# Kernel optimization log

Hardware: AMD Instinct MI355X
Metric: run time of the kernel (lower is better)

Reference implementation:

```python
import jax, jax.numpy as jnp
import numpy as np

B, S, H, NH = 2, 2048, 1024, 16
HD = H // NH


def setup_inputs() -> dict:
    key = jax.random.key(0)
    ks = jax.random.split(key, 14)
    lim = 1.0 / np.sqrt(H)  # torch Linear default init range
    def lin(ka, kb):
        W = jax.random.uniform(ka, (H, H), jnp.float32, -lim, lim)
        b = jax.random.uniform(kb, (H,), jnp.float32, -lim, lim)
        return W, b
    Wq, bq = lin(ks[0], ks[1])
    Wk, bk = lin(ks[2], ks[3])
    Wv, bv = lin(ks[4], ks[5])
    Wo, bo = lin(ks[6], ks[7])
    return {
        "query": jax.random.normal(ks[8], (B, S, H), jnp.float32),
        "key": jax.random.normal(ks[9], (B, S, H), jnp.float32),
        "value": jax.random.normal(ks[10], (B, S, H), jnp.float32),
        "attn_mask": jax.random.randint(ks[11], (B, S, S), 0, 2).astype(bool),
        "relative_time": jax.random.normal(ks[12], (B, 1, S, S), jnp.float32),
        "Wq": Wq, "bq": bq, "Wk": Wk, "bk": bk,
        "Wv": Wv, "bv": bv, "Wo": Wo, "bo": bo,
    }


def reference(query, key, value, attn_mask, relative_time,
              Wq, bq, Wk, bk, Wv, bv, Wo, bo):
    Bq, Sq, _ = query.shape
    Skv = key.shape[1]
    # projections (torch Linear: x @ W^T + b)
    Q = (query @ Wq.T + bq).reshape(Bq, Sq, NH, HD).transpose(0, 2, 1, 3)
    K = (key @ Wk.T + bk).reshape(Bq, Skv, NH, HD).transpose(0, 2, 1, 3)
    V = (value @ Wv.T + bv).reshape(Bq, Skv, NH, HD).transpose(0, 2, 1, 3)
    scale = HD ** (-0.5)
    # NOTE: bias added BEFORE scaling, matching the original (non-standard)
    scores = jnp.einsum("bhqd,bhkd->bhqk", Q, K)
    scores = (scores + relative_time) * scale
    scores = jnp.where(attn_mask[:, None, :, :], scores, -jnp.inf)
    attn = jax.nn.softmax(scores.astype(jnp.float32), axis=-1).astype(scores.dtype)
    attn = jnp.nan_to_num(attn, nan=0.0)
    # dropout is identity in eval mode (dropout_rate applied only when training)
    out = jnp.einsum("bhqk,bhkd->bhqd", attn, V)
    out = out.transpose(0, 2, 1, 3).reshape(Bq, Sq, H)
    return out @ Wo.T + bo
```

## Files before the change

### kernel.cpp

```cpp
#include <hip/hip_runtime.h>
#include <hip/hip_bf16.h>

constexpr int BATCH = 2, SEQ = 2048, HDIM = 1024, NHEADS = 16, HEADD = 64;
constexpr int MROWS = BATCH * SEQ;
constexpr float QSCALE = 0.18033688011112042f;

typedef short short8  __attribute__((ext_vector_type(8)));
typedef float f32x4   __attribute__((ext_vector_type(4)));
typedef float f32x16  __attribute__((ext_vector_type(16)));
typedef int   int4v   __attribute__((ext_vector_type(4)));
typedef unsigned short ushort4v __attribute__((ext_vector_type(4)));

static __device__ __forceinline__ short f2bf(float f) {
    __hip_bfloat16 h = __float2bfloat16(f);
    return *reinterpret_cast<short*>(&h);
}

static __device__ __forceinline__ int cvt_pk_bf16(float a, float b) {
    int r;
    asm("v_cvt_pk_bf16_f32 %0, %1, %2" : "=v"(r) : "v"(a), "v"(b));
    return r;
}

static __device__ __forceinline__ float bfbits2f(unsigned short u) {
    return __builtin_bit_cast(float, (unsigned int)u << 16);
}

static __device__ __forceinline__ void gload_lds16(const void* g, void* l) {
    __builtin_amdgcn_global_load_lds(
        (const __attribute__((address_space(1))) unsigned int*)g,
        (__attribute__((address_space(3))) unsigned int*)l, 16, 0, 0);
}

static __device__ __forceinline__ int swz(int row) {
    return (((row & 7) ^ ((row >> 3) & 3))) << 4;
}

__global__ void cvt_all_kernel(const float* __restrict__ q, const float* __restrict__ k,
                               const float* __restrict__ v, const float* __restrict__ w0,
                               const float* __restrict__ w1, const float* __restrict__ w2,
                               const float* __restrict__ w3,
                               short* __restrict__ xq, short* __restrict__ xk,
                               short* __restrict__ xv, short* __restrict__ o0,
                               short* __restrict__ o1, short* __restrict__ o2,
                               short* __restrict__ o3, int n4x, int n4w) {
    int i = blockIdx.x * blockDim.x + threadIdx.x;
    const int stride = gridDim.x * blockDim.x;
    const int total = 3 * n4x + 4 * n4w;
    for (; i < total; i += stride) {
        const float* in; short* out; int j = i;
        if (j < 3 * n4x) {
            if (j >= 2 * n4x)      { in = v; out = xv; j -= 2 * n4x; }
            else if (j >= n4x)     { in = k; out = xk; j -= n4x; }
            else                   { in = q; out = xq; }
        } else {
            j -= 3 * n4x;
            if (j >= 3 * n4w)      { in = w3; out = o3; j -= 3 * n4w; }
            else if (j >= 2 * n4w) { in = w2; out = o2; j -= 2 * n4w; }
            else if (j >= n4w)     { in = w1; out = o1; j -= n4w; }
            else                   { in = w0; out = o0; }
        }
        const float4 val = reinterpret_cast<const float4*>(in)[j];
        short4 o;
        o.x = f2bf(val.x); o.y = f2bf(val.y); o.z = f2bf(val.z); o.w = f2bf(val.w);
        reinterpret_cast<short4*>(out)[j] = o;
    }
}

__global__ void detect_mask_kernel(const unsigned int* __restrict__ m, int* flag) {
    const int tid = threadIdx.x;
    int gt1 = 0, isf = 0;
    for (int i = 0; i < 4; ++i) {
        unsigned int wv = m[tid + 256 * i];
        if (wv > 1u) gt1 = 1;
        if (wv == 0x3F800000u) isf = 1;
    }
    __shared__ int s_gt1, s_isf;
    if (tid == 0) { s_gt1 = 0; s_isf = 0; }
    __syncthreads();
    if (gt1) atomicOr(&s_gt1, 1);
    if (isf) atomicOr(&s_isf, 1);
    __syncthreads();
    if (tid == 0) flag[0] = s_gt1 ? (s_isf ? 2 : 1) : 0;
}

__global__ void fuse_rel_kernel(const float* __restrict__ rel, const void* __restrict__ mask,
                                const int* __restrict__ flag, short* __restrict__ rT,
                                int nThr) {
    const int f = flag[0];
    int i = blockIdx.x * blockDim.x + threadIdx.x;
    const int stride = gridDim.x * blockDim.x;
    for (; i < nThr; i += stride) {
        const int q    = i & 2047;
        const int kv16 = (i >> 11) & 127;
        const int b    = i >> 18;
        const long base = ((long)(b * 2048 + q)) * 2048 + kv16 * 16;
        float4 rv[4];
        #pragma unroll
        for (int g = 0; g < 4; ++g)
            rv[g] = *reinterpret_cast<const float4*>(rel + base + 4 * g);
        bool mk[16];
        if (f == 1) {
            const unsigned int* mp = (const unsigned int*)((const unsigned char*)mask + base);
            #pragma unroll
            for (int wd = 0; wd < 4; ++wd) {
                const unsigned int mw = mp[wd];
                #pragma unroll
                for (int s = 0; s < 4; ++s) mk[wd * 4 + s] = ((mw >> (8 * s)) & 0xffu) != 0;
            }
        } else if (f == 0) {
            const int* mp = (const int*)mask + base;
            #pragma unroll
            for (int j = 0; j < 16; ++j) mk[j] = mp[j] != 0;
        } else {
            const float* mp = (const float*)mask + base;
            #pragma unroll
            for (int j = 0; j < 16; ++j) mk[j] = mp[j] != 0.0f;
        }
        const float* rp = reinterpret_cast<const float*>(&rv[0]);
        #pragma unroll
        for (int g = 0; g < 4; ++g) {
            short4 o;
            short* op = reinterpret_cast<short*>(&o);
            #pragma unroll
            for (int j = 0; j < 4; ++j) {
                const int idx = 4 * g + j;
                op[j] = f2bf(mk[idx] ? rp[idx] * QSCALE : -1e30f);
            }
            *reinterpret_cast<short4*>(rT + (((long)(b * 512 + kv16 * 4 + g)) * 2048 + q) * 4) = o;
        }
    }
}

template<int BN, typename EPI>
static __device__ __forceinline__
void gemm_core(const short* A, const short* Bw, int K, int m0, int n0, EPI epi) {
    constexpr int NFRAG = BN / 32;
    __shared__ short As[128 * 64];
    __shared__ short Bs[BN * 64];
    const int tid  = threadIdx.x;
    const int lane = tid & 63;
    const int w    = tid >> 6;
    const int lo   = lane & 15, hi = lane >> 4;
    const int wm   = w >> 1, wn = w & 1;

    f32x4 acc[4][NFRAG] = {};

    const int arow  = tid >> 3;
    const int acolb = (tid & 7) * 16;
    const int scolS = acolb ^ swz(arow);
    const char* Ab = (const char*)A + ((long)(m0 + arow) * K) * 2 + scolS;
    const char* Bb = (const char*)Bw + ((long)(n0 + arow) * K) * 2 + scolS;

    for (int k0 = 0; k0 < K; k0 += 64) {
        #pragma unroll
        for (int i = 0; i < 4; ++i)
            gload_lds16(Ab + ((long)i * 32 * K + k0) * 2, (char*)As + i * 4096 + tid * 16);
        #pragma unroll
        for (int i = 0; i < NFRAG; ++i)
            gload_lds16(Bb + ((long)i * 32 * K + k0) * 2, (char*)Bs + i * 4096 + tid * 16);
        __syncthreads();
        #pragma unroll
        for (int ks = 0; ks < 2; ++ks) {
            short8 af[4], bf[NFRAG];
            #pragma unroll
            for (int fm = 0; fm < 4; ++fm) {
                const int row = wm * 64 + fm * 16 + lo;
                af[fm] = *reinterpret_cast<const short8*>(
                    (const char*)As + row * 128 + ((ks * 64 + hi * 16) ^ swz(row)));
            }
            #pragma unroll
            for (int fn = 0; fn < NFRAG; ++fn) {
                const int row = wn * (BN / 2) + fn * 16 + lo;
                bf[fn] = *reinterpret_cast<const short8*>(
                    (const char*)Bs + row * 128 + ((ks * 64 + hi * 16) ^ swz(row)));
            }
            #pragma unroll
            for (int fm = 0; fm < 4; ++fm)
                #pragma unroll
                for (int fn = 0; fn < NFRAG; ++fn)
                    acc[fm][fn] = __builtin_amdgcn_mfma_f32_16x16x32_bf16(
                        af[fm], bf[fn], acc[fm][fn], 0, 0, 0);
        }
        __syncthreads();
    }

    #pragma unroll
    for (int fm = 0; fm < 4; ++fm)
        #pragma unroll
        for (int fn = 0; fn < NFRAG; ++fn) {
            const int n = n0 + wn * (BN / 2) + fn * 16 + lo;
            const int mB = m0 + wm * 64 + fm * 16 + hi * 4;
            for (int r = 0; r < 4; ++r) epi(mB + r, n, acc[fm][fn][r]);
        }
}

__global__ __launch_bounds__(256, 3)
void qkv_gemm(const short* xq, const short* xk, const short* xv,
              const short* wq, const short* wk, const short* wv,
              const float* bq, const float* bk, const float* bv,
              short* Qb, short* Kb, short* Vt) {
    const int which = blockIdx.x >> 8;
    const int bid   = blockIdx.x & 255;
    const int m0 = (bid >> 3) << 7;
    const int n0 = (bid & 7) << 7;
    const short* A    = which == 0 ? xq : which == 1 ? xk : xv;
    const short* W    = which == 0 ? wq : which == 1 ? wk : wv;
    const float* bias = which == 0 ? bq : which == 1 ? bk : bv;
    short* C          = which == 0 ? Qb : which == 1 ? Kb : Vt;
    const float scale = which == 0 ? QSCALE : 1.0f;
    gemm_core<128>(A, W, HDIM, m0, n0, [&](int m, int n, float v) {
        v = (v + bias[n]) * scale;
        const int b = m >> 11, s = m & (SEQ - 1);
        const int h = n >> 6, d = n & 63;
        long idx;
        if (which != 2) idx = (((long)(b * NHEADS + h)) * SEQ + s) * HEADD + d;
        else            idx = (((long)(b * NHEADS + h)) * HEADD + d) * SEQ + s;
        C[idx] = f2bf(v);
    });
}

__global__ __launch_bounds__(256, 2)
void out_gemm(const short* A, const short* W, const float* bias, float* Cout) {
    const int bid = blockIdx.x;
    const int m0 = (bid >> 4) << 7;
    const int n0 = (bid & 15) << 6;
    gemm_core<64>(A, W, HDIM, m0, n0, [&](int m, int n, float v) {
        Cout[(long)m * HDIM + n] = v + bias[n];
    });
}

__global__ __launch_bounds__(256, 4)
void attn_fwd(const short* __restrict__ Qb, const short* __restrict__ Kb,
              const short* __restrict__ Vtb, const short* __restrict__ rT,
              short* __restrict__ Ob) {
    __shared__ short Ks[2][64 * 64];
    __shared__ short Vs[2][64 * 64];
    const int tid  = threadIdx.x;
    const int lane = tid & 63;
    const int wv   = tid >> 6;
    const int qp   = wv & 1;
    const int t    = wv >> 1;
    const int l31  = lane & 31, hi2 = lane >> 5;
    const int wg = ((blockIdx.x & 7) << 7) + (blockIdx.x >> 3);
    const int qt = wg & 31, h = (wg >> 5) & 15, b = wg >> 9;
    const int bh = b * NHEADS + h;
    const int q0 = qt * 64 + qp * 32 + l31;

    short8 qf[4];
    {
        const short* qp_ = Qb + ((long)bh * SEQ + q0) * HEADD + hi2 * 8;
        #pragma unroll
        for (int s = 0; s < 4; ++s)
            qf[s] = *reinterpret_cast<const short8*>(qp_ + s * 16);
    }

    float lsum = 0.0f;
    f32x16 oacc0 = {}, oacc1 = {};

    const int srow  = tid >> 3;
    const int scolb = (tid & 7) * 16;
    const int scolK = scolb ^ swz(srow);
    const char* KbB = (const char*)Kb + ((long)bh * SEQ + srow) * 128 + scolK;
    const char* VbB = (const char*)Vtb + ((long)bh * HEADD + srow) * ((long)SEQ * 2) + scolK;

    auto stage = [&](int buf, int kt) {
        #pragma unroll
        for (int i = 0; i < 2; ++i) {
            gload_lds16(KbB + ((long)kt * 64 + i * 32) * 128,
                        (char*)&Ks[buf][0] + i * 4096 + tid * 16);
            gload_lds16(VbB + (long)i * 32 * (SEQ * 2) + (long)kt * 128,
                        (char*)&Vs[buf][0] + i * 4096 + tid * 16);
        }
    };

    ushort4v rbuf[4];
    auto loadRel = [&](int kt) {
        #pragma unroll
        for (int g = 0; g < 4; ++g) {
            const int p4 = kt * 16 + t * 8 + 2 * g + hi2;
            rbuf[g] = *reinterpret_cast<const ushort4v*>(
                rT + (((long)(b * 512 + p4)) * 2048 + q0) * 4);
        }
    };

    stage(0, 0);
    loadRel(0);

    const int rsw = swz(l31);
    const int NT = SEQ / 64;

    for (int kt = 0; kt < NT; ++kt) {
        const int cb = kt & 1;
        const bool hasNext = (kt < NT - 1);
        if (hasNext) stage(cb ^ 1, kt + 1);
        if (hasNext) asm volatile("s_waitcnt vmcnt(4)" ::: "memory");
        else         asm volatile("s_waitcnt vmcnt(0)" ::: "memory");
        __builtin_amdgcn_s_barrier();
        asm volatile("" ::: "memory");

        f32x16 sc;
        #pragma unroll
        for (int g = 0; g < 4; ++g)
            #pragma unroll
            for (int j = 0; j < 4; ++j)
                sc[4 * g + j] = bfbits2f(rbuf[g][j]);
        if (hasNext) loadRel(kt + 1);

        const char* kls = (const char*)&Ks[cb][0];
        const char* kr  = kls + (t * 32 + l31) * 128;
        __builtin_amdgcn_s_setprio(1);
        #pragma unroll
        for (int s = 0; s < 4; ++s) {
            short8 kf = *reinterpret_cast<const short8*>(kr + ((s * 32 + hi2 * 16) ^ rsw));
            sc = __builtin_amdgcn_mfma_f32_32x32x16_bf16(kf, qf[s], sc, 0, 0, 0);
        }
        __builtin_amdgcn_s_setprio(0);

        int X[8];
        #pragma unroll
        for (int i2 = 0; i2 < 8; ++i2) {
            const float p0 = __builtin_amdgcn_exp2f(sc[2 * i2]);
            const float p1 = __builtin_amdgcn_exp2f(sc[2 * i2 + 1]);
            lsum += p0 + p1;
            X[i2] = cvt_pk_bf16(p0, p1);
        }
        int pa[2][4];
        #pragma unroll
        for (int u = 0; u < 2; ++u) {
            auto r0 = __builtin_amdgcn_permlane32_swap(X[4 * u + 0], X[4 * u + 2], false, false);
            auto r1 = __builtin_amdgcn_permlane32_swap(X[4 * u + 1], X[4 * u + 3], false, false);
            pa[u][0] = (int)r0[0];
            pa[u][1] = (int)r1[0];
            pa[u][2] = (int)r0[1];
            pa[u][3] = (int)r1[1];
        }

        const char* vls = (const char*)&Vs[cb][0];
        __builtin_amdgcn_s_setprio(1);
        #pragma unroll
        for (int dt = 0; dt < 2; ++dt) {
            const char* vr = vls + (dt * 32 + l31) * 128;
            #pragma unroll
            for (int u = 0; u < 2; ++u) {
                const int s = 2 * t + u;
                short8 vf = *reinterpret_cast<const short8*>(vr + ((s * 32 + hi2 * 16) ^ rsw));
                int4v pw = { pa[u][0], pa[u][1], pa[u][2], pa[u][3] };
                if (dt == 0)
                    oacc0 = __builtin_amdgcn_mfma_f32_32x32x16_bf16(
                        __builtin_bit_cast(short8, pw), vf, oacc0, 0, 0, 0);
                else
                    oacc1 = __builtin_amdgcn_mfma_f32_32x32x16_bf16(
                        __builtin_bit_cast(short8, pw), vf, oacc1, 0, 0, 0);
            }
        }
        __builtin_amdgcn_s_setprio(0);

        asm volatile("" ::: "memory");
        __builtin_amdgcn_s_barrier();
    }

    lsum += __shfl_xor(lsum, 32, 64);

    float* cmbO = (float*)&Ks[0][0];
    float* cmbL = (float*)&Vs[0][0];
    if (t == 1) {
        #pragma unroll
        for (int r = 0; r < 16; ++r) {
            const int qloc = (r & 3) + 8 * (r >> 2) + 4 * hi2;
            cmbO[(qp * 32 + qloc) * 64 + l31]      = oacc0[r];
            cmbO[(qp * 32 + qloc) * 64 + 32 + l31] = oacc1[r];
        }
        if (hi2 == 0) cmbL[qp * 32 + l31] = lsum;
    }
    __syncthreads();
    if (t == 0) {
        const float ltot = lsum + cmbL[qp * 32 + l31];
        const float inv  = ltot > 0.0f ? 1.0f / ltot : 0.0f;
        #pragma unroll
        for (int r = 0; r < 16; ++r) {
            const int qloc = (r & 3) + 8 * (r >> 2) + 4 * hi2;
            const float invr = __shfl(inv, qloc, 64);
            const int qg = qt * 64 + qp * 32 + qloc;
            const long obase = ((long)b * SEQ + qg) * HDIM + h * 64 + l31;
            const float o0 = oacc0[r] + cmbO[(qp * 32 + qloc) * 64 + l31];
            const float o1 = oacc1[r] + cmbO[(qp * 32 + qloc) * 64 + 32 + l31];
            Ob[obase]      = f2bf(o0 * invr);
            Ob[obase + 32] = f2bf(o1 * invr);
        }
    }
}

extern "C" void kernel_launch(void* const* d_in, const int* in_sizes, int n_in,
                              void* d_out, int out_size, void* d_ws, size_t ws_size,
                              hipStream_t stream) {
    const float* q    = (const float*)d_in[0];
    const float* k    = (const float*)d_in[1];
    const float* v    = (const float*)d_in[2];
    const void*  mask = d_in[3];
    const float* rel  = (const float*)d_in[4];
    const float* Wq   = (const float*)d_in[5];
    const float* bq   = (const float*)d_in[6];
    const float* Wk   = (const float*)d_in[7];
    const float* bk   = (const float*)d_in[8];
    const float* Wv   = (const float*)d_in[9];
    const float* bv   = (const float*)d_in[10];
    const float* Wo   = (const float*)d_in[11];
    const float* bo   = (const float*)d_in[12];
    (void)in_sizes; (void)n_in; (void)out_size; (void)ws_size;

    char* ws = (char*)d_ws;
    size_t off = 0;
    auto alloc = [&](size_t bytes) {
        char* p = ws + off;
        off += (bytes + 255) & ~(size_t)255;
        return p;
    };
    const size_t xBytes = (size_t)MROWS * HDIM * 2;
    const size_t wBytes = (size_t)HDIM * HDIM * 2;
    const size_t poolBytes = 3 * xBytes + 3 * wBytes;

    short* Qb  = (short*)alloc(xBytes);
    short* Kb  = (short*)alloc(xBytes);
    short* Vt  = (short*)alloc(xBytes);
    short* wob = (short*)alloc(wBytes);
    int*   flag = (int*)alloc(256);
    char* pool = (char*)alloc(poolBytes);
    short* Ab  = (short*)alloc(xBytes);

    short* xq  = (short*)(pool);
    short* xk  = (short*)(pool + xBytes);
    short* xv  = (short*)(pool + 2 * xBytes);
    short* wqb = (short*)(pool + 3 * xBytes);
    short* wkb = (short*)(pool + 3 * xBytes + wBytes);
    short* wvb = (short*)(pool + 3 * xBytes + 2 * wBytes);
    short* rT  = (short*)(pool);

    const int n4x = MROWS * HDIM / 4, n4w = HDIM * HDIM / 4;
    cvt_all_kernel<<<2048, 256, 0, stream>>>(q, k, v, Wq, Wk, Wv, Wo,
                                             xq, xk, xv, wqb, wkb, wvb, wob, n4x, n4w);
    detect_mask_kernel<<<1, 256, 0, stream>>>((const unsigned int*)mask, flag);

    qkv_gemm<<<768, 256, 0, stream>>>(xq, xk, xv, wqb, wkb, wvb,
                                      bq, bk, bv, Qb, Kb, Vt);

    const int relThr = BATCH * 128 * 2048;
    fuse_rel_kernel<<<2048, 256, 0, stream>>>(rel, mask, flag, rT, relThr);

    attn_fwd<<<1024, 256, 0, stream>>>(Qb, Kb, Vt, rT, Ab);

    out_gemm<<<512, 256, 0, stream>>>(Ab, wob, bo, (float*)d_out);
}
```

Baseline: 157.9 us.

## Fuse fp32-to-bf16 conversion into GEMM loads and restructure attention pipeline

Drops the separate conversion kernel. The QKV and output GEMMs now read fp32 activations and weights directly and pack them to bf16 in registers before storing to LDS, which removes one full pass over the inputs and weights. It also remaps block IDs to group tiles across XCDs and raises attn_fwd occupancy to 5. The attention loop is unrolled by two with double-buffered relative-bias registers and one fewer barrier per step. The trade-off is that the GEMMs now use synchronous fp32 global loads instead of direct-to-LDS loads, and each weight tile is converted repeatedly across blocks.

```diff
diff --git a/kernel.cpp b/kernel.cpp
--- a/kernel.cpp
+++ b/kernel.cpp
@@ -34,37 +34,6 @@
 
 static __device__ __forceinline__ int swz(int row) {
     return (((row & 7) ^ ((row >> 3) & 3))) << 4;
-}
-
-__global__ void cvt_all_kernel(const float* __restrict__ q, const float* __restrict__ k,
-                               const float* __restrict__ v, const float* __restrict__ w0,
-                               const float* __restrict__ w1, const float* __restrict__ w2,
-                               const float* __restrict__ w3,
-                               short* __restrict__ xq, short* __restrict__ xk,
-                               short* __restrict__ xv, short* __restrict__ o0,
-                               short* __restrict__ o1, short* __restrict__ o2,
-                               short* __restrict__ o3, int n4x, int n4w) {
-    int i = blockIdx.x * blockDim.x + threadIdx.x;
-    const int stride = gridDim.x * blockDim.x;
-    const int total = 3 * n4x + 4 * n4w;
-    for (; i < total; i += stride) {
-        const float* in; short* out; int j = i;
-        if (j < 3 * n4x) {
-            if (j >= 2 * n4x)      { in = v; out = xv; j -= 2 * n4x; }
-            else if (j >= n4x)     { in = k; out = xk; j -= n4x; }
-            else                   { in = q; out = xq; }
-        } else {
-            j -= 3 * n4x;
-            if (j >= 3 * n4w)      { in = w3; out = o3; j -= 3 * n4w; }
-            else if (j >= 2 * n4w) { in = w2; out = o2; j -= 2 * n4w; }
-            else if (j >= n4w)     { in = w1; out = o1; j -= n4w; }
-            else                   { in = w0; out = o0; }
-        }
-        const float4 val = reinterpret_cast<const float4*>(in)[j];
-        short4 o;
-        o.x = f2bf(val.x); o.y = f2bf(val.y); o.z = f2bf(val.z); o.w = f2bf(val.w);
-        reinterpret_cast<short4*>(out)[j] = o;
-    }
 }
 
 __global__ void detect_mask_kernel(const unsigned int* __restrict__ m, int* flag) {
@@ -132,9 +101,9 @@
     }
 }
 
-template<int BN, typename EPI>
+template<int BN, bool AF32, bool BF32, typename EPI>
 static __device__ __forceinline__
-void gemm_core(const short* A, const short* Bw, int K, int m0, int n0, EPI epi) {
+void gemm_core(const void* A, const void* Bw, int K, int m0, int n0, EPI epi) {
     constexpr int NFRAG = BN / 32;
     __shared__ short As[128 * 64];
     __shared__ short Bs[BN * 64];
@@ -147,18 +116,41 @@
     f32x4 acc[4][NFRAG] = {};
 
     const int arow  = tid >> 3;
-    const int acolb = (tid & 7) * 16;
-    const int scolS = acolb ^ swz(arow);
-    const char* Ab = (const char*)A + ((long)(m0 + arow) * K) * 2 + scolS;
-    const char* Bb = (const char*)Bw + ((long)(n0 + arow) * K) * 2 + scolS;
+    const int kcolB = (tid & 7) * 16;
+    const int scolB = kcolB ^ swz(arow);
+    const int scolE = scolB >> 1;
 
     for (int k0 = 0; k0 < K; k0 += 64) {
         #pragma unroll
-        for (int i = 0; i < 4; ++i)
-            gload_lds16(Ab + ((long)i * 32 * K + k0) * 2, (char*)As + i * 4096 + tid * 16);
-        #pragma unroll
-        for (int i = 0; i < NFRAG; ++i)
-            gload_lds16(Bb + ((long)i * 32 * K + k0) * 2, (char*)Bs + i * 4096 + tid * 16);
+        for (int i = 0; i < 4; ++i) {
+            const int row = i * 32 + arow;
+            char* dst = (char*)As + i * 4096 + tid * 16;
+            if constexpr (AF32) {
+                const float* s = (const float*)A + (long)(m0 + row) * K + k0 + scolE;
+                const float4 v0 = *reinterpret_cast<const float4*>(s);
+                const float4 v1 = *reinterpret_cast<const float4*>(s + 4);
+                int4v pk = { cvt_pk_bf16(v0.x, v0.y), cvt_pk_bf16(v0.z, v0.w),
+                             cvt_pk_bf16(v1.x, v1.y), cvt_pk_bf16(v1.z, v1.w) };
+                *reinterpret_cast<int4v*>(dst) = pk;
+            } else {
+                gload_lds16((const char*)A + ((long)(m0 + row) * K + k0) * 2 + scolB, dst);
+            }
+        }
+        #pragma unroll
+        for (int i = 0; i < NFRAG; ++i) {
+            const int row = i * 32 + arow;
+            char* dst = (char*)Bs + i * 4096 + tid * 16;
+            if constexpr (BF32) {
+                const float* s = (const float*)Bw + (long)(n0 + row) * K + k0 + scolE;
+                const float4 v0 = *reinterpret_cast<const float4*>(s);
+                const float4 v1 = *reinterpret_cast<const float4*>(s + 4);
+                int4v pk = { cvt_pk_bf16(v0.x, v0.y), cvt_pk_bf16(v0.z, v0.w),
+                             cvt_pk_bf16(v1.x, v1.y), cvt_pk_bf16(v1.z, v1.w) };
+                *reinterpret_cast<int4v*>(dst) = pk;
+            } else {
+                gload_lds16((const char*)Bw + ((long)(n0 + row) * K + k0) * 2 + scolB, dst);
+            }
+        }
         __syncthreads();
         #pragma unroll
         for (int ks = 0; ks < 2; ++ks) {
@@ -196,41 +188,42 @@
 }
 
 __global__ __launch_bounds__(256, 3)
-void qkv_gemm(const short* xq, const short* xk, const short* xv,
-              const short* wq, const short* wk, const short* wv,
+void qkv_gemm(const float* q, const float* k, const float* v,
+              const float* Wq, const float* Wk, const float* Wv,
               const float* bq, const float* bk, const float* bv,
               short* Qb, short* Kb, short* Vt) {
-    const int which = blockIdx.x >> 8;
-    const int bid   = blockIdx.x & 255;
+    const int wg    = ((blockIdx.x & 7) * 96) + (blockIdx.x >> 3);
+    const int which = wg >> 8;
+    const int bid   = wg & 255;
     const int m0 = (bid >> 3) << 7;
     const int n0 = (bid & 7) << 7;
-    const short* A    = which == 0 ? xq : which == 1 ? xk : xv;
-    const short* W    = which == 0 ? wq : which == 1 ? wk : wv;
+    const float* A    = which == 0 ? q  : which == 1 ? k  : v;
+    const float* W    = which == 0 ? Wq : which == 1 ? Wk : Wv;
     const float* bias = which == 0 ? bq : which == 1 ? bk : bv;
     short* C          = which == 0 ? Qb : which == 1 ? Kb : Vt;
     const float scale = which == 0 ? QSCALE : 1.0f;
-    gemm_core<128>(A, W, HDIM, m0, n0, [&](int m, int n, float v) {
-        v = (v + bias[n]) * scale;
+    gemm_core<128, true, true>(A, W, HDIM, m0, n0, [&](int m, int n, float val) {
+        val = (val + bias[n]) * scale;
         const int b = m >> 11, s = m & (SEQ - 1);
         const int h = n >> 6, d = n & 63;
         long idx;
         if (which != 2) idx = (((long)(b * NHEADS + h)) * SEQ + s) * HEADD + d;
         else            idx = (((long)(b * NHEADS + h)) * HEADD + d) * SEQ + s;
-        C[idx] = f2bf(v);
+        C[idx] = f2bf(val);
     });
 }
 
 __global__ __launch_bounds__(256, 2)
-void out_gemm(const short* A, const short* W, const float* bias, float* Cout) {
-    const int bid = blockIdx.x;
-    const int m0 = (bid >> 4) << 7;
-    const int n0 = (bid & 15) << 6;
-    gemm_core<64>(A, W, HDIM, m0, n0, [&](int m, int n, float v) {
+void out_gemm(const short* A, const float* W, const float* bias, float* Cout) {
+    const int wg = ((blockIdx.x & 7) * 64) + (blockIdx.x >> 3);
+    const int m0 = (wg >> 4) << 7;
+    const int n0 = (wg & 15) << 6;
+    gemm_core<64, false, true>(A, W, HDIM, m0, n0, [&](int m, int n, float v) {
         Cout[(long)m * HDIM + n] = v + bias[n];
     });
 }
 
-__global__ __launch_bounds__(256, 4)
+__global__ __launch_bounds__(256, 5)
 void attn_fwd(const short* __restrict__ Qb, const short* __restrict__ Kb,
               const short* __restrict__ Vtb, const short* __restrict__ rT,
               short* __restrict__ Ob) {
@@ -274,93 +267,98 @@
         }
     };
 
-    ushort4v rbuf[4];
-    auto loadRel = [&](int kt) {
+    ushort4v rbA[4], rbB[4];
+    const short* rTb = rT + ((long)b * 512 * 2048 + (long)q0) * 4;
+    auto loadRel = [&](ushort4v* rb, int kt) {
         #pragma unroll
         for (int g = 0; g < 4; ++g) {
             const int p4 = kt * 16 + t * 8 + 2 * g + hi2;
-            rbuf[g] = *reinterpret_cast<const ushort4v*>(
-                rT + (((long)(b * 512 + p4)) * 2048 + q0) * 4);
+            rb[g] = *reinterpret_cast<const ushort4v*>(rTb + (long)p4 * 2048 * 4);
         }
     };
 
     stage(0, 0);
-    loadRel(0);
+    loadRel(rbA, 0);
+    loadRel(rbB, 1);
 
     const int rsw = swz(l31);
     const int NT = SEQ / 64;
 
-    for (int kt = 0; kt < NT; ++kt) {
-        const int cb = kt & 1;
-        const bool hasNext = (kt < NT - 1);
-        if (hasNext) stage(cb ^ 1, kt + 1);
-        if (hasNext) asm volatile("s_waitcnt vmcnt(4)" ::: "memory");
-        else         asm volatile("s_waitcnt vmcnt(0)" ::: "memory");
-        __builtin_amdgcn_s_barrier();
-        asm volatile("" ::: "memory");
-
-        f32x16 sc;
-        #pragma unroll
-        for (int g = 0; g < 4; ++g)
-            #pragma unroll
-            for (int j = 0; j < 4; ++j)
-                sc[4 * g + j] = bfbits2f(rbuf[g][j]);
-        if (hasNext) loadRel(kt + 1);
-
-        const char* kls = (const char*)&Ks[cb][0];
-        const char* kr  = kls + (t * 32 + l31) * 128;
-        __builtin_amdgcn_s_setprio(1);
-        #pragma unroll
-        for (int s = 0; s < 4; ++s) {
-            short8 kf = *reinterpret_cast<const short8*>(kr + ((s * 32 + hi2 * 16) ^ rsw));
-            sc = __builtin_amdgcn_mfma_f32_32x32x16_bf16(kf, qf[s], sc, 0, 0, 0);
-        }
-        __builtin_amdgcn_s_setprio(0);
-
-        int X[8];
-        #pragma unroll
-        for (int i2 = 0; i2 < 8; ++i2) {
-            const float p0 = __builtin_amdgcn_exp2f(sc[2 * i2]);
-            const float p1 = __builtin_amdgcn_exp2f(sc[2 * i2 + 1]);
-            lsum += p0 + p1;
-            X[i2] = cvt_pk_bf16(p0, p1);
-        }
-        int pa[2][4];
-        #pragma unroll
-        for (int u = 0; u < 2; ++u) {
-            auto r0 = __builtin_amdgcn_permlane32_swap(X[4 * u + 0], X[4 * u + 2], false, false);
-            auto r1 = __builtin_amdgcn_permlane32_swap(X[4 * u + 1], X[4 * u + 3], false, false);
-            pa[u][0] = (int)r0[0];
-            pa[u][1] = (int)r1[0];
-            pa[u][2] = (int)r0[1];
-            pa[u][3] = (int)r1[1];
-        }
-
-        const char* vls = (const char*)&Vs[cb][0];
-        __builtin_amdgcn_s_setprio(1);
-        #pragma unroll
-        for (int dt = 0; dt < 2; ++dt) {
-            const char* vr = vls + (dt * 32 + l31) * 128;
+    #pragma unroll 1
+    for (int kt = 0; kt < NT; kt += 2) {
+        #pragma unroll
+        for (int half = 0; half < 2; ++half) {
+            const int ki = kt + half;
+            const int cb = ki & 1;
+            const ushort4v* rb = half == 0 ? rbA : rbB;
+            const bool tailWait = (ki + 2 >= NT) && (half == 1);
+            if (tailWait) asm volatile("s_waitcnt vmcnt(0)" ::: "memory");
+            else          asm volatile("s_waitcnt vmcnt(4)" ::: "memory");
+            __builtin_amdgcn_s_barrier();
+            asm volatile("" ::: "memory");
+            if (ki + 1 < NT) stage(cb ^ 1, ki + 1);
+
+            f32x16 sc;
+            #pragma unroll
+            for (int g = 0; g < 4; ++g)
+                #pragma unroll
+                for (int j = 0; j < 4; ++j)
+                    sc[4 * g + j] = bfbits2f(rb[g][j]);
+            if (ki + 2 < NT) loadRel(half == 0 ? rbA : rbB, ki + 2);
+
+            const char* kr = (const char*)&Ks[cb][0] + (t * 32 + l31) * 128;
+            __builtin_amdgcn_s_setprio(1);
+            #pragma unroll
+            for (int s = 0; s < 4; ++s) {
+                short8 kf = *reinterpret_cast<const short8*>(kr + ((s * 32 + hi2 * 16) ^ rsw));
+                sc = __builtin_amdgcn_mfma_f32_32x32x16_bf16(kf, qf[s], sc, 0, 0, 0);
+            }
+            __builtin_amdgcn_s_setprio(0);
+
+            int X[8];
+            #pragma unroll
+            for (int i2 = 0; i2 < 8; ++i2) {
+                const float p0 = __builtin_amdgcn_exp2f(sc[2 * i2]);
+                const float p1 = __builtin_amdgcn_exp2f(sc[2 * i2 + 1]);
+                lsum += p0 + p1;
+                X[i2] = cvt_pk_bf16(p0, p1);
+            }
+            int pa[2][4];
             #pragma unroll
             for (int u = 0; u < 2; ++u) {
-                const int s = 2 * t + u;
-                short8 vf = *reinterpret_cast<const short8*>(vr + ((s * 32 + hi2 * 16) ^ rsw));
-                int4v pw = { pa[u][0], pa[u][1], pa[u][2], pa[u][3] };
-                if (dt == 0)
-                    oacc0 = __builtin_amdgcn_mfma_f32_32x32x16_bf16(
-                        __builtin_bit_cast(short8, pw), vf, oacc0, 0, 0, 0);
-                else
-                    oacc1 = __builtin_amdgcn_mfma_f32_32x32x16_bf16(
-                        __builtin_bit_cast(short8, pw), vf, oacc1, 0, 0, 0);
-            }
-        }
-        __builtin_amdgcn_s_setprio(0);
-
-        asm volatile("" ::: "memory");
-        __builtin_amdgcn_s_barrier();
+                auto r0 = __builtin_amdgcn_permlane32_swap(X[4 * u + 0], X[4 * u + 2], false, false);
+                auto r1 = __builtin_amdgcn_permlane32_swap(X[4 * u + 1], X[4 * u + 3], false, false);
+                pa[u][0] = (int)r0[0];
+                pa[u][1] = (int)r1[0];
+                pa[u][2] = (int)r0[1];
+                pa[u][3] = (int)r1[1];
+            }
+
+            const char* vls = (const char*)&Vs[cb][0];
+            __builtin_amdgcn_s_setprio(1);
+            #pragma unroll
+            for (int dt = 0; dt < 2; ++dt) {
+                const char* vr = vls + (dt * 32 + l31) * 128;
+                #pragma unroll
+                for (int u = 0; u < 2; ++u) {
+                    const int s = 2 * t + u;
+                    short8 vf = *reinterpret_cast<const short8*>(vr + ((s * 32 + hi2 * 16) ^ rsw));
+                    int4v pw = { pa[u][0], pa[u][1], pa[u][2], pa[u][3] };
+                    if (dt == 0)
+                        oacc0 = __builtin_amdgcn_mfma_f32_32x32x16_bf16(
+                            __builtin_bit_cast(short8, pw), vf, oacc0, 0, 0, 0);
+                    else
+                        oacc1 = __builtin_amdgcn_mfma_f32_32x32x16_bf16(
+                            __builtin_bit_cast(short8, pw), vf, oacc1, 0, 0, 0);
+                }
+            }
+            __builtin_amdgcn_s_setprio(0);
+        }
     }
 
     lsum += __shfl_xor(lsum, 32, 64);
+
+    __syncthreads();
 
     float* cmbO = (float*)&Ks[0][0];
     float* cmbL = (float*)&Vs[0][0];
@@ -416,32 +414,19 @@
         off += (bytes + 255) & ~(size_t)255;
         return p;
     };
-    const size_t xBytes = (size_t)MROWS * HDIM * 2;
-    const size_t wBytes = (size_t)HDIM * HDIM * 2;
-    const size_t poolBytes = 3 * xBytes + 3 * wBytes;
+    const size_t xBytes  = (size_t)MROWS * HDIM * 2;
+    const size_t rtBytes = (size_t)BATCH * 2048 * 2048 * 2;
 
     short* Qb  = (short*)alloc(xBytes);
     short* Kb  = (short*)alloc(xBytes);
     short* Vt  = (short*)alloc(xBytes);
-    short* wob = (short*)alloc(wBytes);
+    short* Ab  = (short*)alloc(xBytes);
+    short* rT  = (short*)alloc(rtBytes);
     int*   flag = (int*)alloc(256);
-    char* pool = (char*)alloc(poolBytes);
-    short* Ab  = (short*)alloc(xBytes);
-
-    short* xq  = (short*)(pool);
-    short* xk  = (short*)(pool + xBytes);
-    short* xv  = (short*)(pool + 2 * xBytes);
-    short* wqb = (short*)(pool + 3 * xBytes);
-    short* wkb = (short*)(pool + 3 * xBytes + wBytes);
-    short* wvb = (short*)(pool + 3 * xBytes + 2 * wBytes);
-    short* rT  = (short*)(pool);
-
-    const int n4x = MROWS * HDIM / 4, n4w = HDIM * HDIM / 4;
-    cvt_all_kernel<<<2048, 256, 0, stream>>>(q, k, v, Wq, Wk, Wv, Wo,
-                                             xq, xk, xv, wqb, wkb, wvb, wob, n4x, n4w);
+
     detect_mask_kernel<<<1, 256, 0, stream>>>((const unsigned int*)mask, flag);
 
-    qkv_gemm<<<768, 256, 0, stream>>>(xq, xk, xv, wqb, wkb, wvb,
+    qkv_gemm<<<768, 256, 0, stream>>>(q, k, v, Wq, Wk, Wv,
                                       bq, bk, bv, Qb, Kb, Vt);
 
     const int relThr = BATCH * 128 * 2048;
@@ -449,5 +434,5 @@
 
     attn_fwd<<<1024, 256, 0, stream>>>(Qb, Kb, Vt, rT, Ab);
 
-    out_gemm<<<512, 256, 0, stream>>>(Ab, wob, bo, (float*)d_out);
-}
+    out_gemm<<<512, 256, 0, stream>>>(Ab, Wo, bo, (float*)d_out);
+}
```

Result: slower. 331.4 us (+109.8%).
